# Kernel optimization log

Measured on AMD Instinct MI355X. Metric: run time of the kernel, lower is better.

The kernel has to match this reference:

```python
import jax, jax.numpy as jnp
import numpy as np

MAT_DIM = 4  # quaternion algebra vector size
EMBED_DIM = 1024
NUM_HEADS = 16
HEAD_DIM = EMBED_DIM // NUM_HEADS  # 64
SCALE = 1.0 / np.sqrt(HEAD_DIM)


def quaternion_structure():
    # C[i,j,k]: e_i * e_j = sum_k C[i,j,k] e_k, basis (1, i, j, k)
    C = np.zeros((4, 4, 4), dtype=np.float32)
    table = [
        (0, 0, 0, 1.0), (0, 1, 1, 1.0), (0, 2, 2, 1.0), (0, 3, 3, 1.0),
        (1, 0, 1, 1.0), (2, 0, 2, 1.0), (3, 0, 3, 1.0),
        (1, 1, 0, -1.0), (2, 2, 0, -1.0), (3, 3, 0, -1.0),
        (1, 2, 3, 1.0), (2, 1, 3, -1.0),
        (2, 3, 1, 1.0), (3, 2, 1, -1.0),
        (3, 1, 2, 1.0), (1, 3, 2, -1.0),
    ]
    for i, j, k, s in table:
        C[i, j, k] = s
    return jnp.asarray(C)


def algebra_linear(x, W, b, C):
    # x: [B,S,Nin,d] algebra-blocked input; W: [Nout,Nin,d]; b: [Nout,d]
    # y[b,s,o,k] = sum_{n,i,j} C[i,j,k] W[o,n,i] x[b,s,n,j] + b[o,k]
    Wm = jnp.einsum('oni,ijk->onjk', W, C)  # left-multiplication matrices
    return jnp.einsum('bsnj,onjk->bsok', x, Wm) + b


def setup_inputs() -> dict:
    key = jax.random.key(0)
    ks = jax.random.split(key, 6)
    B, S = 2, 2048
    nb = EMBED_DIM // MAT_DIM  # 256 algebra blocks
    w_std = 0.02
    inp = {
        'x': jax.random.normal(ks[0], (B, S, EMBED_DIM), dtype=jnp.float32),
        'mask': jnp.ones((1, 1, S, S), dtype=jnp.int32),
        'Wq': jax.random.normal(ks[1], (nb, nb, MAT_DIM), dtype=jnp.float32) * w_std,
        'bq': jnp.zeros((nb, MAT_DIM), dtype=jnp.float32),
        'Wk': jax.random.normal(ks[2], (nb, nb, MAT_DIM), dtype=jnp.float32) * w_std,
        'bk': jnp.zeros((nb, MAT_DIM), dtype=jnp.float32),
        'Wv': jax.random.normal(ks[3], (nb, nb, MAT_DIM), dtype=jnp.float32) * w_std,
        'bv': jnp.zeros((nb, MAT_DIM), dtype=jnp.float32),
        'Wo': jax.random.normal(ks[4], (nb, nb, MAT_DIM), dtype=jnp.float32) * w_std,
        'bo': jnp.zeros((nb, MAT_DIM), dtype=jnp.float32),
    }
    return inp


def reference(x, mask, Wq, bq, Wk, bk, Wv, bv, Wo, bo):
    C = quaternion_structure()
    B, S, E = x.shape
    xb = x.reshape(B, S, E // MAT_DIM, MAT_DIM)

    q = algebra_linear(xb, Wq, bq, C).reshape(B, S, E)
    k = algebra_linear(xb, Wk, bk, C).reshape(B, S, E)
    v = algebra_linear(xb, Wv, bv, C).reshape(B, S, E)

    def split_heads(t):  # [B,S,E] -> [B,H,S,hd]
        return t.reshape(B, S, NUM_HEADS, HEAD_DIM).transpose(0, 2, 1, 3)

    q, k, v = split_heads(q), split_heads(k), split_heads(v)

    scores = jnp.einsum('bhqd,bhkd->bhqk', q, k) * SCALE
    scores = jnp.where(mask == 0, -jnp.inf, scores)
    attn = jax.nn.softmax(scores, axis=-1)
    context = jnp.einsum('bhqk,bhkd->bhqd', attn, v)
    context = context.transpose(0, 2, 1, 3).reshape(B, S, E)

    cb = context.reshape(B, S, E // MAT_DIM, MAT_DIM)
    out = algebra_linear(cb, Wo, bo, C).reshape(B, S, E)
    return out
```

## Files before the change

kernel.cpp:

```cpp
#include <hip/hip_runtime.h>
#include <hip/hip_bf16.h>

typedef __attribute__((ext_vector_type(8))) short bf16x8;
typedef __attribute__((ext_vector_type(4))) float f32x4;
typedef __attribute__((ext_vector_type(8))) float f32x8;
typedef __attribute__((ext_vector_type(16))) float f32x16;
typedef __attribute__((ext_vector_type(4))) unsigned short u16x4;
typedef __attribute__((ext_vector_type(4))) unsigned int u32x4;
typedef __attribute__((ext_vector_type(2))) unsigned int u32x2;

#define LOG2E 1.4426950408889634f
#define SCLOG 0.18033688011118312f
#define EXP2(x) __builtin_amdgcn_exp2f(x)

static __device__ __forceinline__ unsigned short f2bf(float f) {
  __hip_bfloat16 h = __float2bfloat16(f);
  return __builtin_bit_cast(unsigned short, h);
}
static __device__ __forceinline__ float bf2f(unsigned short u) {
  __hip_bfloat16 h = __builtin_bit_cast(__hip_bfloat16, u);
  return __bfloat162float(h);
}
static __device__ __forceinline__ unsigned cvtpk(float lo, float hg) {
  unsigned r;
  asm("v_cvt_pk_bf16_f32 %0, %1, %2" : "=v"(r) : "v"(lo), "v"(hg));
  return r;
}
static __device__ __forceinline__ bf16x8 ld16(const void* p) {
  return *(const bf16x8*)p;
}
static __device__ __forceinline__ void gload16(const void* g, void* l) {
  __builtin_amdgcn_global_load_lds(
      (const __attribute__((address_space(1))) void*)g,
      (__attribute__((address_space(3))) void*)l, 16, 0, 0);
}

__global__ void prep(const float* __restrict__ x,
                     const int* __restrict__ mask,
                     const float* __restrict__ Wq,
                     const float* __restrict__ Wk,
                     const float* __restrict__ Wv,
                     const float* __restrict__ Wo,
                     unsigned short* __restrict__ xb,
                     unsigned short* __restrict__ Mqkv,
                     unsigned short* __restrict__ Mo,
                     unsigned long long* __restrict__ bits_t)
{
  const int bx = blockIdx.x, tid = threadIdx.x;
  if (bx < 16384) {
    const int g = bx * 256 + tid;
    const unsigned long long w = __ballot(mask[g] != 0);
    if ((tid & 63) == 0) {
      const int idx = g >> 6;
      const int sq = idx >> 5, kw = idx & 31;
      bits_t[(size_t)kw * 2048 + sq] = w;
    }
  } else if (bx < 20480) {
    const int i = (bx - 16384) * 256 + tid;
    const float4 a = ((const float4*)x)[i];
    u32x2 o; o[0] = cvtpk(a.x, a.y); o[1] = cvtpk(a.z, a.w);
    ((u32x2*)xb)[i] = o;
  } else {
    const int e = bx - 20480;
    const int mat = e >> 8;
    const int o = e & 255;
    const int n = tid;
    const float* W = (mat == 0) ? Wq : (mat == 1) ? Wk : (mat == 2) ? Wv : Wo;
    unsigned short* M = (mat < 3) ? (Mqkv + (size_t)mat * 1024 * 1024) : Mo;
    const float4 w = *(const float4*)(W + ((size_t)o * 256 + n) * 4);
    const unsigned short w0 = f2bf(w.x), w1 = f2bf(w.y), w2 = f2bf(w.z), w3 = f2bf(w.w);
#define NG(u) ((unsigned short)((u) ^ 0x8000))
    u16x4 r0; r0[0] = w0;     r0[1] = NG(w1); r0[2] = NG(w2); r0[3] = NG(w3);
    u16x4 r1; r1[0] = w1;     r1[1] = w0;     r1[2] = NG(w3); r1[3] = w2;
    u16x4 r2; r2[0] = w2;     r2[1] = w3;     r2[2] = w0;     r2[3] = NG(w1);
    u16x4 r3; r3[0] = w3;     r3[1] = NG(w2); r3[2] = w1;     r3[3] = w0;
#undef NG
    unsigned short* dst = M + (size_t)(o * 4) * 1024 + n * 4;
    *(u16x4*)(dst)        = r0;
    *(u16x4*)(dst + 1024) = r1;
    *(u16x4*)(dst + 2048) = r2;
    *(u16x4*)(dst + 3072) = r3;
  }
}

template <int MODE, int BM>
__global__ __launch_bounds__(256, 3)
void gemm_bt(const unsigned short* __restrict__ A,
             const unsigned short* __restrict__ Bm,
             const float* __restrict__ bias0,
             const float* __restrict__ bias1,
             const float* __restrict__ bias2,
             unsigned short* __restrict__ out0,
             unsigned short* __restrict__ out1,
             unsigned short* __restrict__ out2,
             float* __restrict__ fout)
{
  constexpr int K = 1024;
  constexpr int FR = BM / 32;
  __shared__ unsigned short As[BM * 64];
  __shared__ unsigned short Bs[128 * 64];
  const int tid = threadIdx.x;
  const int lane = tid & 63;
  const int wave = tid >> 6;
  const int bn = blockIdx.x, bm = blockIdx.y;
  const int wm = wave >> 1, wn = wave & 1;
  const int l15 = lane & 15, l4 = lane >> 4;

  f32x4 zero4 = {0.f, 0.f, 0.f, 0.f};
  f32x4 acc[FR][4];
#pragma unroll
  for (int i = 0; i < FR; ++i)
#pragma unroll
    for (int j = 0; j < 4; ++j) acc[i][j] = zero4;

  for (int kk = 0; kk < K; kk += 64) {
#pragma unroll
    for (int c = 0; c < BM / 32; ++c) {
      const int Lb = (wave * (BM / 32) + c) * 1024;
      const int L = Lb + lane * 16;
      const int row = L >> 7;
      const int slot = (L >> 4) & 7;
      const int ss = slot ^ (row & 7);
      gload16(A + (size_t)(bm * BM + row) * K + kk + ss * 8, (char*)As + Lb);
    }
#pragma unroll
    for (int c = 0; c < 4; ++c) {
      const int Lb = (wave * 4 + c) * 1024;
      const int L = Lb + lane * 16;
      const int row = L >> 7;
      const int slot = (L >> 4) & 7;
      const int ss = slot ^ (row & 7);
      gload16(Bm + (size_t)(bn * 128 + row) * K + kk + ss * 8, (char*)Bs + Lb);
    }
    __syncthreads();
#pragma unroll
    for (int ks = 0; ks < 2; ++ks) {
      bf16x8 af[FR], bfr[4];
#pragma unroll
      for (int i = 0; i < FR; ++i) {
        const int ra = wm * (BM / 2) + i * 16 + l15;
        const int sa = (ks * 4 + l4) ^ (ra & 7);
        af[i] = ld16((const char*)As + ra * 128 + sa * 16);
      }
#pragma unroll
      for (int j = 0; j < 4; ++j) {
        const int rb = wn * 64 + j * 16 + l15;
        const int sb = (ks * 4 + l4) ^ (rb & 7);
        bfr[j] = ld16((const char*)Bs + rb * 128 + sb * 16);
      }
#pragma unroll
      for (int i = 0; i < FR; ++i)
#pragma unroll
        for (int j = 0; j < 4; ++j)
          acc[i][j] = __builtin_amdgcn_mfma_f32_16x16x32_bf16(af[i], bfr[j], acc[i][j], 0, 0, 0);
    }
    __syncthreads();
  }

#pragma unroll
  for (int i = 0; i < FR; ++i) {
    const int t0 = bm * BM + wm * (BM / 2) + i * 16 + l4 * 4;
#pragma unroll
    for (int j = 0; j < 4; ++j) {
      const int e = bn * 128 + wn * 64 + j * 16 + l15;
      f32x4 v = acc[i][j];
      if (MODE == 0) {
        const int which = e >> 10;
        const int e1 = e & 1023;
        const float* bp = (which == 0) ? bias0 : (which == 1 ? bias1 : bias2);
        const float bias = bp[e1];
        if (which == 0) {
#pragma unroll
          for (int r = 0; r < 4; ++r)
            out0[(size_t)(t0 + r) * 1024 + e1] = f2bf((v[r] + bias) * SCLOG);
        } else if (which == 1) {
#pragma unroll
          for (int r = 0; r < 4; ++r)
            out1[(size_t)(t0 + r) * 1024 + e1] = f2bf(v[r] + bias);
        } else {
          const int h = e1 >> 6, d = e1 & 63;
          const int b = t0 >> 11, s = t0 & 2047;
          u16x4 pk;
#pragma unroll
          for (int r = 0; r < 4; ++r) pk[r] = f2bf(v[r] + bias);
          *(u16x4*)&out2[((size_t)((b * 16 + h) * 64 + d)) * 2048 + s] = pk;
        }
      } else {
        const float bias = bias0[e];
#pragma unroll
        for (int r = 0; r < 4; ++r)
          fout[(size_t)(t0 + r) * 1024 + e] = v[r] + bias;
      }
    }
  }
}

__global__ __launch_bounds__(256, 2)
void attn_fwd(const unsigned short* __restrict__ q,
              const unsigned short* __restrict__ k,
              const unsigned short* __restrict__ vt,
              const unsigned long long* __restrict__ mbt,
              unsigned short* __restrict__ po,
              float* __restrict__ sbuf)
{
  constexpr int S = 2048;
  __shared__ __align__(16) unsigned short Ks[2 * 4096];
  __shared__ __align__(16) unsigned short Vs[2 * 4096];

  const int bid = blockIdx.x;
  const int vb = (bid & 7) * 64 + (bid >> 3);
  const int half = vb & 1;
  const int qg = (vb >> 1) & 7;
  const int bh = vb >> 4;
  const int b = bh >> 4, h = bh & 15;

  const int tid = threadIdx.x, lane = tid & 63, wave = tid >> 6;
  const int l31 = lane & 31, hif = lane >> 5;
  const int sq0 = qg * 256 + wave * 64 + l31;
  const int sq1 = sq0 + 32;
  const size_t gq0 = (size_t)b * S + sq0;
  const size_t gq1 = (size_t)b * S + sq1;

  bf16x8 bqfA[4], bqfB[4];
#pragma unroll
  for (int s = 0; s < 4; ++s) {
    bqfA[s] = ld16(q + gq0 * 1024 + h * 64 + s * 16 + hif * 8);
    bqfB[s] = ld16(q + gq1 * 1024 + h * 64 + s * 16 + hif * 8);
  }

  f32x16 o00 = {}, o01 = {}, o10 = {}, o11 = {};
  f32x8 lA8 = {}, lB8 = {};
  const int k0 = half * 16;

#define STAGE(bufi, kti)                                                                  \
  {                                                                                       \
    _Pragma("unroll")                                                                     \
    for (int c = 0; c < 2; ++c) {                                                         \
      const int sl = c * 256 + tid;                                                       \
      const int row = sl >> 3;                                                            \
      const int ss = (sl & 7) ^ (row & 7);                                                \
      gload16(k + (size_t)(b * S + (kti) * 64 + row) * 1024 + h * 64 + ss * 8,            \
              (char*)Ks + (bufi) * 8192 + (c * 4 + wave) * 1024);                         \
      gload16(vt + (size_t)(bh * 64 + row) * 2048 + (kti) * 64 + ss * 8,                  \
              (char*)Vs + (bufi) * 8192 + (c * 4 + wave) * 1024);                         \
    }                                                                                     \
  }

  STAGE(0, k0);
  __syncthreads();

  int buf = 0;
  for (int kt = k0; kt < k0 + 16; ++kt) {
    const unsigned long long w0 = mbt[(size_t)kt * 2048 + sq0];
    const unsigned long long w1 = mbt[(size_t)kt * 2048 + sq1];
    if (kt + 1 < k0 + 16) STAGE(buf ^ 1, kt + 1);

    const char* Kb = (const char*)Ks + buf * 8192;
    const char* Vb = (const char*)Vs + buf * 8192;

    const int kr0 = l31, kr1 = 32 + l31;
    bf16x8 ak0[4], ak1[4];
#pragma unroll
    for (int s = 0; s < 4; ++s) {
      ak0[s] = ld16(Kb + kr0 * 128 + (((s * 2 + hif) ^ (kr0 & 7)) << 4));
      ak1[s] = ld16(Kb + kr1 * 128 + (((s * 2 + hif) ^ (kr1 & 7)) << 4));
    }

    f32x16 pA0 = {}, pB0 = {}, pA1 = {}, pB1 = {};
    __builtin_amdgcn_s_setprio(1);
#pragma unroll
    for (int s = 0; s < 4; ++s) {
      pA0 = __builtin_amdgcn_mfma_f32_32x32x16_bf16(ak0[s], bqfA[s], pA0, 0, 0, 0);
      pB0 = __builtin_amdgcn_mfma_f32_32x32x16_bf16(ak0[s], bqfB[s], pB0, 0, 0, 0);
      pA1 = __builtin_amdgcn_mfma_f32_32x32x16_bf16(ak1[s], bqfA[s], pA1, 0, 0, 0);
      pB1 = __builtin_amdgcn_mfma_f32_32x32x16_bf16(ak1[s], bqfB[s], pB1, 0, 0, 0);
    }
    __builtin_amdgcn_s_setprio(0);

    const unsigned wA0 = (unsigned)w0, wA1 = (unsigned)(w0 >> 32);
    const unsigned wB0 = (unsigned)w1, wB1 = (unsigned)(w1 >> 32);
    if (!__all((wA0 & wA1 & wB0 & wB1) == 0xffffffffu)) {
#pragma unroll
      for (int c = 0; c < 16; ++c) {
        const int key = (c & 3) + 8 * (c >> 2) + 4 * hif;
        if (!((wA0 >> key) & 1u)) pA0[c] = -INFINITY;
        if (!((wA1 >> key) & 1u)) pA1[c] = -INFINITY;
        if (!((wB0 >> key) & 1u)) pB0[c] = -INFINITY;
        if (!((wB1 >> key) & 1u)) pB1[c] = -INFINITY;
      }
    }

#pragma unroll
    for (int c = 0; c < 16; ++c) {
      pA0[c] = EXP2(pA0[c]); pA1[c] = EXP2(pA1[c]);
      pB0[c] = EXP2(pB0[c]); pB1[c] = EXP2(pB1[c]);
    }

#pragma unroll
    for (int c = 0; c < 8; ++c) {
      lA8[c] += (pA0[c] + pA0[c + 8]) + (pA1[c] + pA1[c + 8]);
      lB8[c] += (pB0[c] + pB0[c + 8]) + (pB1[c] + pB1[c + 8]);
    }

    u32x4 bpwA[4], bpwB[4];
#pragma unroll
    for (int sub = 0; sub < 2; ++sub) {
      const f32x16 psA = sub ? pA1 : pA0;
      const f32x16 psB = sub ? pB1 : pB0;
#pragma unroll
      for (int ks = 0; ks < 2; ++ks) {
        const int rb2 = ks * 8;
        const int fi = sub * 2 + ks;
        unsigned XA0 = cvtpk(psA[rb2 + 0], psA[rb2 + 1]);
        unsigned XA1 = cvtpk(psA[rb2 + 2], psA[rb2 + 3]);
        unsigned YA0 = cvtpk(psA[rb2 + 4], psA[rb2 + 5]);
        unsigned YA1 = cvtpk(psA[rb2 + 6], psA[rb2 + 7]);
        asm("v_permlane32_swap_b32 %0, %1" : "+v"(XA0), "+v"(YA0));
        asm("v_permlane32_swap_b32 %0, %1" : "+v"(XA1), "+v"(YA1));
        bpwA[fi][0] = XA0; bpwA[fi][1] = XA1; bpwA[fi][2] = YA0; bpwA[fi][3] = YA1;
        unsigned XB0 = cvtpk(psB[rb2 + 0], psB[rb2 + 1]);
        unsigned XB1 = cvtpk(psB[rb2 + 2], psB[rb2 + 3]);
        unsigned YB0 = cvtpk(psB[rb2 + 4], psB[rb2 + 5]);
        unsigned YB1 = cvtpk(psB[rb2 + 6], psB[rb2 + 7]);
        asm("v_permlane32_swap_b32 %0, %1" : "+v"(XB0), "+v"(YB0));
        asm("v_permlane32_swap_b32 %0, %1" : "+v"(XB1), "+v"(YB1));
        bpwB[fi][0] = XB0; bpwB[fi][1] = XB1; bpwB[fi][2] = YB0; bpwB[fi][3] = YB1;
      }
    }

    __builtin_amdgcn_s_setprio(1);
#pragma unroll
    for (int fi = 0; fi < 4; ++fi) {
      const int slot = fi * 2 + hif;
      const int r0 = l31, r1 = 32 + l31;
      bf16x8 v0 = ld16(Vb + r0 * 128 + ((slot ^ (r0 & 7)) << 4));
      bf16x8 v1 = ld16(Vb + r1 * 128 + ((slot ^ (r1 & 7)) << 4));
      const bf16x8 fA = __builtin_bit_cast(bf16x8, bpwA[fi]);
      const bf16x8 fB = __builtin_bit_cast(bf16x8, bpwB[fi]);
      o00 = __builtin_amdgcn_mfma_f32_32x32x16_bf16(v0, fA, o00, 0, 0, 0);
      o01 = __builtin_amdgcn_mfma_f32_32x32x16_bf16(v1, fA, o01, 0, 0, 0);
      o10 = __builtin_amdgcn_mfma_f32_32x32x16_bf16(v0, fB, o10, 0, 0, 0);
      o11 = __builtin_amdgcn_mfma_f32_32x32x16_bf16(v1, fB, o11, 0, 0, 0);
    }
    __builtin_amdgcn_s_setprio(0);

    __syncthreads();
    buf ^= 1;
  }
#undef STAGE

  float tA[4], tB[4];
#pragma unroll
  for (int c = 0; c < 4; ++c) { tA[c] = lA8[c] + lA8[c + 4]; tB[c] = lB8[c] + lB8[c + 4]; }
  float lA = (tA[0] + tA[1]) + (tA[2] + tA[3]);
  float lB = (tB[0] + tB[1]) + (tB[2] + tB[3]);
  lA += __shfl_xor(lA, 32, 64);
  lB += __shfl_xor(lB, 32, 64);

  const float invA = (lA > 0.f) ? 1.f / lA : 0.f;
  const float invB = (lB > 0.f) ? 1.f / lB : 0.f;
  const float sA = (lA > 0.f) ? __log2f(lA) : -1e30f;
  const float sB = (lB > 0.f) ? __log2f(lB) : -1e30f;
  unsigned short* cpA = po + ((size_t)(half * 32 + bh) * 2048 + sq0) * 64;
  unsigned short* cpB = po + ((size_t)(half * 32 + bh) * 2048 + sq1) * 64;
#pragma unroll
  for (int g = 0; g < 4; ++g) {
    u32x2 a0, a1, b0, b1;
    a0[0] = cvtpk(o00[g * 4 + 0] * invA, o00[g * 4 + 1] * invA);
    a0[1] = cvtpk(o00[g * 4 + 2] * invA, o00[g * 4 + 3] * invA);
    a1[0] = cvtpk(o01[g * 4 + 0] * invA, o01[g * 4 + 1] * invA);
    a1[1] = cvtpk(o01[g * 4 + 2] * invA, o01[g * 4 + 3] * invA);
    b0[0] = cvtpk(o10[g * 4 + 0] * invB, o10[g * 4 + 1] * invB);
    b0[1] = cvtpk(o10[g * 4 + 2] * invB, o10[g * 4 + 3] * invB);
    b1[0] = cvtpk(o11[g * 4 + 0] * invB, o11[g * 4 + 1] * invB);
    b1[1] = cvtpk(o11[g * 4 + 2] * invB, o11[g * 4 + 3] * invB);
    *(u32x2*)(cpA + g * 8 + hif * 4) = a0;
    *(u32x2*)(cpA + 32 + g * 8 + hif * 4) = a1;
    *(u32x2*)(cpB + g * 8 + hif * 4) = b0;
    *(u32x2*)(cpB + 32 + g * 8 + hif * 4) = b1;
  }
  if (hif == 0) {
    sbuf[half * 65536 + bh * 2048 + sq0] = sA;
    sbuf[half * 65536 + bh * 2048 + sq1] = sB;
  }
}

__global__ void merge_halves(const unsigned short* __restrict__ po,
                             const float* __restrict__ sbuf,
                             unsigned short* __restrict__ ctx)
{
  const int t = blockIdx.x * 256 + threadIdx.x;
  const int row = t >> 3;
  const int d0 = (t & 7) * 8;
  const int bh = row >> 11, sq = row & 2047;
  const int b = bh >> 4, h = bh & 15;

  const float s0 = sbuf[row];
  const float s1 = sbuf[65536 + row];
  const bf16x8 a = ld16(po + (size_t)row * 64 + d0);
  const bf16x8 c = ld16(po + 4194304 + (size_t)row * 64 + d0);
  const float smax = fmaxf(s0, s1);
  float w0 = EXP2(s0 - smax), w1 = EXP2(s1 - smax);
  const float winv = 1.f / (w0 + w1);
  w0 *= winv; w1 *= winv;

  float f[8];
#pragma unroll
  for (int j = 0; j < 8; ++j)
    f[j] = w0 * bf2f((unsigned short)a[j]) + w1 * bf2f((unsigned short)c[j]);
  u32x4 r;
  r[0] = cvtpk(f[0], f[1]);
  r[1] = cvtpk(f[2], f[3]);
  r[2] = cvtpk(f[4], f[5]);
  r[3] = cvtpk(f[6], f[7]);
  *(u32x4*)(ctx + ((size_t)b * 2048 + sq) * 1024 + h * 64 + d0) = r;
}

extern "C" void kernel_launch(void* const* d_in, const int* in_sizes, int n_in,
                              void* d_out, int out_size, void* d_ws, size_t ws_size,
                              hipStream_t stream)
{
  const float* x  = (const float*)d_in[0];
  const int* mask = (const int*)d_in[1];
  const float* Wq = (const float*)d_in[2];
  const float* bq = (const float*)d_in[3];
  const float* Wk = (const float*)d_in[4];
  const float* bk = (const float*)d_in[5];
  const float* Wv = (const float*)d_in[6];
  const float* bv = (const float*)d_in[7];
  const float* Wo = (const float*)d_in[8];
  const float* bo = (const float*)d_in[9];

  char* ws = (char*)d_ws;
  unsigned short* Mqkv = (unsigned short*)(ws);
  unsigned short* Mo   = (unsigned short*)(ws + (6ull  << 20));
  unsigned short* xb   = (unsigned short*)(ws + (8ull  << 20));
  unsigned short* ctx  = (unsigned short*)(ws + (8ull  << 20));
  unsigned short* qb_  = (unsigned short*)(ws + (16ull << 20));
  unsigned short* kb_  = (unsigned short*)(ws + (24ull << 20));
  unsigned short* vtb  = (unsigned short*)(ws + (32ull << 20));
  unsigned long long* bits = (unsigned long long*)(ws + (40ull << 20));
  float* sbuf = (float*)(ws + (40ull << 20) + (512ull << 10));
  unsigned short* po = (unsigned short*)d_out;

  prep<<<dim3(21504), 256, 0, stream>>>(x, mask, Wq, Wk, Wv, Wo, xb, Mqkv, Mo, bits);
  gemm_bt<0, 128><<<dim3(24, 32), 256, 0, stream>>>(xb, Mqkv, bq, bk, bv, qb_, kb_, vtb, nullptr);
  attn_fwd<<<dim3(512), 256, 0, stream>>>(qb_, kb_, vtb, bits, po, sbuf);
  merge_halves<<<dim3(2048), 256, 0, stream>>>(po, sbuf, ctx);
  gemm_bt<1, 64><<<dim3(8, 64), 256, 0, stream>>>(ctx, Mo, bo, bo, bo, nullptr, nullptr, nullptr,
                                                  (float*)d_out);
}
```

Before: 111.5 us.

## Process two key tiles per barrier with quad-buffered LDS and new swizzle

The attention loop now stages two 64-key tiles per iteration into a four-slot LDS ring and computes both before a single barrier. This halves the number of __syncthreads calls and deepens the prefetch. The LDS swizzle also now mixes row bits 3-4 into the slot XOR, aimed at reducing bank conflicts. The s_setprio hints around the MFMA blocks are removed. LDS use doubles to 64KB per block, which may limit occupancy at the requested two blocks per CU.

Result: slower. 130.6 us (+17.1%).

```diff
diff --git a/kernel.cpp b/kernel.cpp
--- a/kernel.cpp
+++ b/kernel.cpp
@@ -12,6 +12,7 @@
 #define LOG2E 1.4426950408889634f
 #define SCLOG 0.18033688011118312f
 #define EXP2(x) __builtin_amdgcn_exp2f(x)
+#define SWZ(r) (((r) & 7) ^ (((r) >> 3) & 3))
 
 static __device__ __forceinline__ unsigned short f2bf(float f) {
   __hip_bfloat16 h = __float2bfloat16(f);
@@ -204,8 +205,8 @@
               float* __restrict__ sbuf)
 {
   constexpr int S = 2048;
-  __shared__ __align__(16) unsigned short Ks[2 * 4096];
-  __shared__ __align__(16) unsigned short Vs[2 * 4096];
+  __shared__ __align__(16) unsigned short Ks[4 * 4096];
+  __shared__ __align__(16) unsigned short Vs[4 * 4096];
 
   const int bid = blockIdx.x;
   const int vb = (bid & 7) * 64 + (bid >> 3);
@@ -238,7 +239,7 @@
     for (int c = 0; c < 2; ++c) {                                                         \
       const int sl = c * 256 + tid;                                                       \
       const int row = sl >> 3;                                                            \
-      const int ss = (sl & 7) ^ (row & 7);                                                \
+      const int ss = (sl & 7) ^ SWZ(row);                                                 \
       gload16(k + (size_t)(b * S + (kti) * 64 + row) * 1024 + h * 64 + ss * 8,            \
               (char*)Ks + (bufi) * 8192 + (c * 4 + wave) * 1024);                         \
       gload16(vt + (size_t)(bh * 64 + row) * 2048 + (kti) * 64 + ss * 8,                  \
@@ -246,108 +247,108 @@
     }                                                                                     \
   }
 
+#define COMPUTE(bufi, w0, w1)                                                             \
+  {                                                                                       \
+    const char* Kb = (const char*)Ks + (bufi) * 8192;                                     \
+    const char* Vb = (const char*)Vs + (bufi) * 8192;                                     \
+    const int kr0 = l31, kr1 = 32 + l31;                                                  \
+    bf16x8 ak0[4], ak1[4];                                                                \
+    _Pragma("unroll")                                                                     \
+    for (int s = 0; s < 4; ++s) {                                                         \
+      ak0[s] = ld16(Kb + kr0 * 128 + (((s * 2 + hif) ^ SWZ(kr0)) << 4));                  \
+      ak1[s] = ld16(Kb + kr1 * 128 + (((s * 2 + hif) ^ SWZ(kr1)) << 4));                  \
+    }                                                                                     \
+    f32x16 pA0 = {}, pB0 = {}, pA1 = {}, pB1 = {};                                        \
+    _Pragma("unroll")                                                                     \
+    for (int s = 0; s < 4; ++s) {                                                         \
+      pA0 = __builtin_amdgcn_mfma_f32_32x32x16_bf16(ak0[s], bqfA[s], pA0, 0, 0, 0);       \
+      pB0 = __builtin_amdgcn_mfma_f32_32x32x16_bf16(ak0[s], bqfB[s], pB0, 0, 0, 0);       \
+      pA1 = __builtin_amdgcn_mfma_f32_32x32x16_bf16(ak1[s], bqfA[s], pA1, 0, 0, 0);       \
+      pB1 = __builtin_amdgcn_mfma_f32_32x32x16_bf16(ak1[s], bqfB[s], pB1, 0, 0, 0);       \
+    }                                                                                     \
+    const unsigned wA0 = (unsigned)(w0), wA1 = (unsigned)((w0) >> 32);                    \
+    const unsigned wB0 = (unsigned)(w1), wB1 = (unsigned)((w1) >> 32);                    \
+    if (!__all((wA0 & wA1 & wB0 & wB1) == 0xffffffffu)) {                                 \
+      _Pragma("unroll")                                                                   \
+      for (int c = 0; c < 16; ++c) {                                                      \
+        const int key = (c & 3) + 8 * (c >> 2) + 4 * hif;                                 \
+        if (!((wA0 >> key) & 1u)) pA0[c] = -INFINITY;                                     \
+        if (!((wA1 >> key) & 1u)) pA1[c] = -INFINITY;                                     \
+        if (!((wB0 >> key) & 1u)) pB0[c] = -INFINITY;                                     \
+        if (!((wB1 >> key) & 1u)) pB1[c] = -INFINITY;                                     \
+      }                                                                                   \
+    }                                                                                     \
+    _Pragma("unroll")                                                                     \
+    for (int c = 0; c < 16; ++c) {                                                        \
+      pA0[c] = EXP2(pA0[c]); pA1[c] = EXP2(pA1[c]);                                       \
+      pB0[c] = EXP2(pB0[c]); pB1[c] = EXP2(pB1[c]);                                       \
+    }                                                                                     \
+    _Pragma("unroll")                                                                     \
+    for (int c = 0; c < 8; ++c) {                                                         \
+      lA8[c] += (pA0[c] + pA0[c + 8]) + (pA1[c] + pA1[c + 8]);                            \
+      lB8[c] += (pB0[c] + pB0[c + 8]) + (pB1[c] + pB1[c + 8]);                            \
+    }                                                                                     \
+    u32x4 bpwA[4], bpwB[4];                                                               \
+    _Pragma("unroll")                                                                     \
+    for (int sub = 0; sub < 2; ++sub) {                                                   \
+      const f32x16 psA = sub ? pA1 : pA0;                                                 \
+      const f32x16 psB = sub ? pB1 : pB0;                                                 \
+      _Pragma("unroll")                                                                   \
+      for (int ks = 0; ks < 2; ++ks) {                                                    \
+        const int rb2 = ks * 8;                                                           \
+        const int fi = sub * 2 + ks;                                                      \
+        unsigned XA0 = cvtpk(psA[rb2 + 0], psA[rb2 + 1]);                                 \
+        unsigned XA1 = cvtpk(psA[rb2 + 2], psA[rb2 + 3]);                                 \
+        unsigned YA0 = cvtpk(psA[rb2 + 4], psA[rb2 + 5]);                                 \
+        unsigned YA1 = cvtpk(psA[rb2 + 6], psA[rb2 + 7]);                                 \
+        asm("v_permlane32_swap_b32 %0, %1" : "+v"(XA0), "+v"(YA0));                       \
+        asm("v_permlane32_swap_b32 %0, %1" : "+v"(XA1), "+v"(YA1));                       \
+        bpwA[fi][0] = XA0; bpwA[fi][1] = XA1; bpwA[fi][2] = YA0; bpwA[fi][3] = YA1;       \
+        unsigned XB0 = cvtpk(psB[rb2 + 0], psB[rb2 + 1]);                                 \
+        unsigned XB1 = cvtpk(psB[rb2 + 2], psB[rb2 + 3]);                                 \
+        unsigned YB0 = cvtpk(psB[rb2 + 4], psB[rb2 + 5]);                                 \
+        unsigned YB1 = cvtpk(psB[rb2 + 6], psB[rb2 + 7]);                                 \
+        asm("v_permlane32_swap_b32 %0, %1" : "+v"(XB0), "+v"(YB0));                       \
+        asm("v_permlane32_swap_b32 %0, %1" : "+v"(XB1), "+v"(YB1));                       \
+        bpwB[fi][0] = XB0; bpwB[fi][1] = XB1; bpwB[fi][2] = YB0; bpwB[fi][3] = YB1;       \
+      }                                                                                   \
+    }                                                                                     \
+    _Pragma("unroll")                                                                     \
+    for (int fi = 0; fi < 4; ++fi) {                                                      \
+      const int slot = fi * 2 + hif;                                                      \
+      const int r0 = l31, r1 = 32 + l31;                                                  \
+      bf16x8 v0 = ld16(Vb + r0 * 128 + ((slot ^ SWZ(r0)) << 4));                          \
+      bf16x8 v1 = ld16(Vb + r1 * 128 + ((slot ^ SWZ(r1)) << 4));                          \
+      const bf16x8 fA = __builtin_bit_cast(bf16x8, bpwA[fi]);                             \
+      const bf16x8 fB = __builtin_bit_cast(bf16x8, bpwB[fi]);                             \
+      o00 = __builtin_amdgcn_mfma_f32_32x32x16_bf16(v0, fA, o00, 0, 0, 0);                \
+      o01 = __builtin_amdgcn_mfma_f32_32x32x16_bf16(v1, fA, o01, 0, 0, 0);                \
+      o10 = __builtin_amdgcn_mfma_f32_32x32x16_bf16(v0, fB, o10, 0, 0, 0);                \
+      o11 = __builtin_amdgcn_mfma_f32_32x32x16_bf16(v1, fB, o11, 0, 0, 0);                \
+    }                                                                                     \
+  }
+
   STAGE(0, k0);
+  STAGE(1, k0 + 1);
   __syncthreads();
 
-  int buf = 0;
-  for (int kt = k0; kt < k0 + 16; ++kt) {
-    const unsigned long long w0 = mbt[(size_t)kt * 2048 + sq0];
-    const unsigned long long w1 = mbt[(size_t)kt * 2048 + sq1];
-    if (kt + 1 < k0 + 16) STAGE(buf ^ 1, kt + 1);
-
-    const char* Kb = (const char*)Ks + buf * 8192;
-    const char* Vb = (const char*)Vs + buf * 8192;
-
-    const int kr0 = l31, kr1 = 32 + l31;
-    bf16x8 ak0[4], ak1[4];
-#pragma unroll
-    for (int s = 0; s < 4; ++s) {
-      ak0[s] = ld16(Kb + kr0 * 128 + (((s * 2 + hif) ^ (kr0 & 7)) << 4));
-      ak1[s] = ld16(Kb + kr1 * 128 + (((s * 2 + hif) ^ (kr1 & 7)) << 4));
-    }
-
-    f32x16 pA0 = {}, pB0 = {}, pA1 = {}, pB1 = {};
-    __builtin_amdgcn_s_setprio(1);
-#pragma unroll
-    for (int s = 0; s < 4; ++s) {
-      pA0 = __builtin_amdgcn_mfma_f32_32x32x16_bf16(ak0[s], bqfA[s], pA0, 0, 0, 0);
-      pB0 = __builtin_amdgcn_mfma_f32_32x32x16_bf16(ak0[s], bqfB[s], pB0, 0, 0, 0);
-      pA1 = __builtin_amdgcn_mfma_f32_32x32x16_bf16(ak1[s], bqfA[s], pA1, 0, 0, 0);
-      pB1 = __builtin_amdgcn_mfma_f32_32x32x16_bf16(ak1[s], bqfB[s], pB1, 0, 0, 0);
-    }
-    __builtin_amdgcn_s_setprio(0);
-
-    const unsigned wA0 = (unsigned)w0, wA1 = (unsigned)(w0 >> 32);
-    const unsigned wB0 = (unsigned)w1, wB1 = (unsigned)(w1 >> 32);
-    if (!__all((wA0 & wA1 & wB0 & wB1) == 0xffffffffu)) {
-#pragma unroll
-      for (int c = 0; c < 16; ++c) {
-        const int key = (c & 3) + 8 * (c >> 2) + 4 * hif;
-        if (!((wA0 >> key) & 1u)) pA0[c] = -INFINITY;
-        if (!((wA1 >> key) & 1u)) pA1[c] = -INFINITY;
-        if (!((wB0 >> key) & 1u)) pB0[c] = -INFINITY;
-        if (!((wB1 >> key) & 1u)) pB1[c] = -INFINITY;
-      }
-    }
-
-#pragma unroll
-    for (int c = 0; c < 16; ++c) {
-      pA0[c] = EXP2(pA0[c]); pA1[c] = EXP2(pA1[c]);
-      pB0[c] = EXP2(pB0[c]); pB1[c] = EXP2(pB1[c]);
-    }
-
-#pragma unroll
-    for (int c = 0; c < 8; ++c) {
-      lA8[c] += (pA0[c] + pA0[c + 8]) + (pA1[c] + pA1[c + 8]);
-      lB8[c] += (pB0[c] + pB0[c + 8]) + (pB1[c] + pB1[c + 8]);
-    }
-
-    u32x4 bpwA[4], bpwB[4];
-#pragma unroll
-    for (int sub = 0; sub < 2; ++sub) {
-      const f32x16 psA = sub ? pA1 : pA0;
-      const f32x16 psB = sub ? pB1 : pB0;
-#pragma unroll
-      for (int ks = 0; ks < 2; ++ks) {
-        const int rb2 = ks * 8;
-        const int fi = sub * 2 + ks;
-        unsigned XA0 = cvtpk(psA[rb2 + 0], psA[rb2 + 1]);
-        unsigned XA1 = cvtpk(psA[rb2 + 2], psA[rb2 + 3]);
-        unsigned YA0 = cvtpk(psA[rb2 + 4], psA[rb2 + 5]);
-        unsigned YA1 = cvtpk(psA[rb2 + 6], psA[rb2 + 7]);
-        asm("v_permlane32_swap_b32 %0, %1" : "+v"(XA0), "+v"(YA0));
-        asm("v_permlane32_swap_b32 %0, %1" : "+v"(XA1), "+v"(YA1));
-        bpwA[fi][0] = XA0; bpwA[fi][1] = XA1; bpwA[fi][2] = YA0; bpwA[fi][3] = YA1;
-        unsigned XB0 = cvtpk(psB[rb2 + 0], psB[rb2 + 1]);
-        unsigned XB1 = cvtpk(psB[rb2 + 2], psB[rb2 + 3]);
-        unsigned YB0 = cvtpk(psB[rb2 + 4], psB[rb2 + 5]);
-        unsigned YB1 = cvtpk(psB[rb2 + 6], psB[rb2 + 7]);
-        asm("v_permlane32_swap_b32 %0, %1" : "+v"(XB0), "+v"(YB0));
-        asm("v_permlane32_swap_b32 %0, %1" : "+v"(XB1), "+v"(YB1));
-        bpwB[fi][0] = XB0; bpwB[fi][1] = XB1; bpwB[fi][2] = YB0; bpwB[fi][3] = YB1;
-      }
-    }
-
-    __builtin_amdgcn_s_setprio(1);
-#pragma unroll
-    for (int fi = 0; fi < 4; ++fi) {
-      const int slot = fi * 2 + hif;
-      const int r0 = l31, r1 = 32 + l31;
-      bf16x8 v0 = ld16(Vb + r0 * 128 + ((slot ^ (r0 & 7)) << 4));
-      bf16x8 v1 = ld16(Vb + r1 * 128 + ((slot ^ (r1 & 7)) << 4));
-      const bf16x8 fA = __builtin_bit_cast(bf16x8, bpwA[fi]);
-      const bf16x8 fB = __builtin_bit_cast(bf16x8, bpwB[fi]);
-      o00 = __builtin_amdgcn_mfma_f32_32x32x16_bf16(v0, fA, o00, 0, 0, 0);
-      o01 = __builtin_amdgcn_mfma_f32_32x32x16_bf16(v1, fA, o01, 0, 0, 0);
-      o10 = __builtin_amdgcn_mfma_f32_32x32x16_bf16(v0, fB, o10, 0, 0, 0);
-      o11 = __builtin_amdgcn_mfma_f32_32x32x16_bf16(v1, fB, o11, 0, 0, 0);
-    }
-    __builtin_amdgcn_s_setprio(0);
-
+  for (int ktp = 0; ktp < 8; ++ktp) {
+    const int kt = k0 + ktp * 2;
+    const int pair = ktp & 1;
+    const unsigned long long w0a = mbt[(size_t)kt * 2048 + sq0];
+    const unsigned long long w1a = mbt[(size_t)kt * 2048 + sq1];
+    const unsigned long long w0b = mbt[(size_t)(kt + 1) * 2048 + sq0];
+    const unsigned long long w1b = mbt[(size_t)(kt + 1) * 2048 + sq1];
+    if (ktp < 7) {
+      STAGE((pair ^ 1) * 2 + 0, kt + 2);
+      STAGE((pair ^ 1) * 2 + 1, kt + 3);
+    }
+    COMPUTE(pair * 2 + 0, w0a, w1a);
+    COMPUTE(pair * 2 + 1, w0b, w1b);
     __syncthreads();
-    buf ^= 1;
   }
 #undef STAGE
+#undef COMPUTE
 
   float tA[4], tB[4];
 #pragma unroll
```
